# Optimization experiments

Measured on AMD Instinct MI355X. Metric: run time of the kernel, lower is better.

Reference implementation:

```python
import jax, jax.numpy as jnp
import numpy as np

N_NODES = 100000
N_EDGES = 1600000
IN_FEATS = 64
OUT_FEATS = 64
BN_EPS = 1e-5


def setup_inputs() -> dict:
    key = jax.random.key(0)
    ks = jax.random.split(key, 5)
    feats = jax.random.normal(ks[0], (N_NODES, IN_FEATS), dtype=jnp.float32)
    src = jax.random.randint(ks[1], (N_EDGES,), 0, N_NODES, dtype=jnp.int32)
    dst = jax.random.randint(ks[2], (N_EDGES,), 0, N_NODES, dtype=jnp.int32)
    scale = 1.0 / np.sqrt(IN_FEATS)
    W = jax.random.normal(ks[3], (IN_FEATS, OUT_FEATS), dtype=jnp.float32) * scale
    b = jnp.zeros((OUT_FEATS,), dtype=jnp.float32)
    Wr = jax.random.normal(ks[4], (IN_FEATS, OUT_FEATS), dtype=jnp.float32) * scale
    br = jnp.zeros((OUT_FEATS,), dtype=jnp.float32)
    gamma = jnp.ones((OUT_FEATS,), dtype=jnp.float32)
    beta = jnp.zeros((OUT_FEATS,), dtype=jnp.float32)
    return {"feats": feats, "src": src, "dst": dst, "W": W, "b": b,
            "Wr": Wr, "br": br, "gamma": gamma, "beta": beta}


def reference(feats, src, dst, W, b, Wr, br, gamma, beta):
    N = feats.shape[0]
    # GraphConv(norm='none'): sum-aggregate source features into destinations (SpMM),
    # then linear + bias + activation (relu).
    agg = jax.ops.segment_sum(feats[src], dst, num_segments=N)  # [N, IN]
    h = jax.nn.relu(agg @ W + b)                                # [N, OUT]
    # residual branch: activation(Linear(feats))
    res = jax.nn.relu(feats @ Wr + br)
    h = h + res
    # dropout p=0.0 -> identity
    # BatchNorm1d (training mode): biased variance over node dim, eps=1e-5
    mean = jnp.mean(h, axis=0)
    var = jnp.var(h, axis=0)
    return (h - mean) * jax.lax.rsqrt(var + BN_EPS) * gamma + beta
```

## Files before the change

### kernel.cpp

```cpp
#include <hip/hip_runtime.h>
#include <hip/hip_bf16.h>


typedef __attribute__((ext_vector_type(8))) short short8;
typedef __attribute__((ext_vector_type(4))) float f32x4;

constexpr int BKT  = 128;
constexpr int NBKT_MAX = 1024;
constexpr int SCAP = 3072;
constexpr int PB   = 8192;
constexpr int CAST_BLKS = 2048;

static __device__ __forceinline__ float bfbits_lo(unsigned u) {
    union { unsigned u; float f; } c; c.u = u << 16; return c.f;
}
static __device__ __forceinline__ float bfbits_hi(unsigned u) {
    union { unsigned u; float f; } c; c.u = u & 0xffff0000u; return c.f;
}
static __device__ __forceinline__ short bf16r(float x) {
    __hip_bfloat16 h = __float2bfloat16(x);
    union { __hip_bfloat16 h; short s; } c; c.h = h; return c.s;
}
static __device__ __forceinline__ unsigned bf16pair(float x, float y) {
    return (unsigned)(unsigned short)bf16r(x) | ((unsigned)(unsigned short)bf16r(y) << 16);
}

__global__ __launch_bounds__(256) void k_prep(
    const float* __restrict__ feats, unsigned short* __restrict__ feats_h, int total8,
    const float* __restrict__ W, const float* __restrict__ Wr,
    short* __restrict__ Wpk, short* __restrict__ Wrpk)
{
    const int bid = blockIdx.x;
    if (bid < CAST_BLKS) {
        for (int i = bid * 256 + threadIdx.x; i < total8; i += CAST_BLKS * 256) {
            float4 v0 = ((const float4*)feats)[i * 2];
            float4 v1 = ((const float4*)feats)[i * 2 + 1];
            short8 o;
            o[0] = bf16r(v0.x); o[1] = bf16r(v0.y); o[2] = bf16r(v0.z); o[3] = bf16r(v0.w);
            o[4] = bf16r(v1.x); o[5] = bf16r(v1.y); o[6] = bf16r(v1.z); o[7] = bf16r(v1.w);
            ((short8*)feats_h)[i] = o;
        }
    } else {
        for (int idx = threadIdx.x; idx < 8192; idx += 256) {
            const int m = idx >> 12;
            const int rem = idx & 4095;
            const int j = rem & 7;
            const int q = rem >> 3;
            const int lane = q & 63;
            const int st = q >> 6;
            const int s = st >> 2;
            const int t = st & 3;
            const int k = s * 32 + (lane >> 4) * 8 + j;
            const int n = t * 16 + (lane & 15);
            const float v = (m == 0) ? W[k * 64 + n] : Wr[k * 64 + n];
            short* out = (m == 0) ? Wpk : Wrpk;
            out[rem] = bf16r(v);
        }
    }
}

__global__ __launch_bounds__(1024) void k_part(
    const int* __restrict__ src, const int* __restrict__ dst,
    int* __restrict__ cursor, unsigned* __restrict__ pk_slots,
    int n_edges, int nbkt)
{
    __shared__ unsigned stage[PB];
    __shared__ int hist[NBKT_MAX], lofs[NBKT_MAX], cnt2[NBKT_MAX];
    const int tid = threadIdx.x;
    const int e0 = blockIdx.x * PB;

    for (int i = tid; i < NBKT_MAX; i += 1024) { hist[i] = 0; cnt2[i] = 0; }
    __syncthreads();

    unsigned pk[8]; unsigned short bb8[8];
    #pragma unroll
    for (int i = 0; i < 8; i++) {
        const int e = e0 + i * 1024 + tid;
        if (e < n_edges) {
            const int d = dst[e];
            const int s = src[e];
            const int bb = d >> 7;
            bb8[i] = (unsigned short)bb;
            pk[i] = ((unsigned)(d & 127) << 17) | (unsigned)s;
            atomicAdd(&hist[bb], 1);
        } else bb8[i] = 0xffff;
    }
    __syncthreads();

    int myc = 0, mybase = 0;
    if (tid < nbkt) {
        myc = hist[tid];
        if (myc > 0) mybase = atomicAdd(&cursor[tid], myc);
    }
    const int v = (tid < nbkt) ? myc : 0;
    lofs[tid] = v;
    __syncthreads();
    for (int off = 1; off < 1024; off <<= 1) {
        int x = (tid >= off) ? lofs[tid - off] : 0;
        __syncthreads();
        lofs[tid] += x;
        __syncthreads();
    }
    const int myex = lofs[tid] - v;
    __syncthreads();
    lofs[tid] = myex;
    __syncthreads();

    #pragma unroll
    for (int i = 0; i < 8; i++) {
        if (bb8[i] != 0xffff) {
            const int spos = lofs[bb8[i]] + atomicAdd(&cnt2[bb8[i]], 1);
            stage[spos] = pk[i];
        }
    }
    __syncthreads();

    if (tid < nbkt && myc > 0) {
        int room = SCAP - mybase;
        const int c = myc < room ? myc : (room > 0 ? room : 0);
        unsigned* gp = pk_slots + (size_t)tid * SCAP + mybase;
        const int lbase = myex;
        for (int j = 0; j < c; j++) gp[j] = stage[lbase + j];
    }
}

__global__ __launch_bounds__(1024) void k_gsort(
    const unsigned short* __restrict__ feats_h, const int* __restrict__ cursor,
    const unsigned* __restrict__ pk_slots, unsigned short* __restrict__ aggh,
    int n_nodes)
{
    __shared__ unsigned raw[SCAP];
    __shared__ unsigned srt[SCAP];
    __shared__ int cnt[BKT], cnt2[BKT], lofs[BKT], noff[BKT + 1];
    const int bkt = blockIdx.x;
    const int tid = threadIdx.x;
    int m = cursor[bkt]; if (m > SCAP) m = SCAP;
    const unsigned* gsl = pk_slots + (size_t)bkt * SCAP;

    if (tid < BKT) { cnt[tid] = 0; cnt2[tid] = 0; }
    __syncthreads();
    for (int i = tid; i < m; i += 1024) {
        const unsigned p = gsl[i];
        raw[i] = p;
        atomicAdd(&cnt[p >> 17], 1);
    }
    __syncthreads();
    if (tid < BKT) lofs[tid] = cnt[tid];
    __syncthreads();
    for (int off = 1; off < BKT; off <<= 1) {
        int x = 0;
        if (tid < BKT && tid >= off) x = lofs[tid - off];
        __syncthreads();
        if (tid < BKT) lofs[tid] += x;
        __syncthreads();
    }
    if (tid < BKT) noff[tid + 1] = lofs[tid];
    if (tid == 0) noff[0] = 0;
    __syncthreads();
    for (int i = tid; i < m; i += 1024) {
        const unsigned p = raw[i];
        const int d = p >> 17;
        const int spos = noff[d] + atomicAdd(&cnt2[d], 1);
        srt[spos] = p & 0x1ffffu;
    }
    __syncthreads();

    const int wave = tid >> 6;
    const int lane = tid & 63;
    const int half = lane >> 5;
    const int li   = lane & 31;
    #pragma unroll 1
    for (int k = 0; k < 8; k++) {
        const int nl = wave * 8 + k;
        const int n  = bkt * BKT + nl;
        if (n >= n_nodes) break;
        const int beg = noff[nl], end = noff[nl + 1];
        float ax0 = 0.f, ax1 = 0.f, ax2 = 0.f, ax3 = 0.f;
        float ay0 = 0.f, ay1 = 0.f, ay2 = 0.f, ay3 = 0.f;
        for (int base = beg; base < end; base += 16) {
            #pragma unroll
            for (int j = 0; j < 8; j++) {
                const int e = base + 2 * j + half;
                const bool vd = e < end;
                const unsigned s = srt[vd ? e : beg];
                const unsigned val = *(const unsigned*)(feats_h + (size_t)s * 64 + li * 2);
                const float flo = vd ? bfbits_lo(val) : 0.f;
                const float fhi = vd ? bfbits_hi(val) : 0.f;
                switch (j & 3) {
                    case 0: ax0 += flo; ay0 += fhi; break;
                    case 1: ax1 += flo; ay1 += fhi; break;
                    case 2: ax2 += flo; ay2 += fhi; break;
                    default: ax3 += flo; ay3 += fhi; break;
                }
            }
        }
        float ax = (ax0 + ax1) + (ax2 + ax3);
        float ay = (ay0 + ay1) + (ay2 + ay3);
        ax += __shfl_xor(ax, 32);
        ay += __shfl_xor(ay, 32);
        if (half == 0)
            *(unsigned*)(aggh + (size_t)n * 128 + li * 2) = bf16pair(ax, ay);
    }
}

__global__ __launch_bounds__(512) void k_mv(
    const unsigned short* aggh, const unsigned short* __restrict__ feats_h,
    const short* __restrict__ Wpk, const short* __restrict__ Wrpk,
    const float* __restrict__ b, const float* __restrict__ br,
    float* h, float* __restrict__ bnacc, int n_nodes)
{
    __shared__ float ssum[64], ssq[64];
    const int tid = threadIdx.x;
    const int wave = tid >> 6;
    const int lane = tid & 63;
    if (tid < 64) { ssum[tid] = 0.f; ssq[tid] = 0.f; }
    __syncthreads();

    short8 wf[8], wrf[8];
    #pragma unroll
    for (int i = 0; i < 8; i++) {
        wf[i]  = *(const short8*)(Wpk  + (i * 64 + lane) * 8);
        wrf[i] = *(const short8*)(Wrpk + (i * 64 + lane) * 8);
    }
    float bt[4], brt[4];
    #pragma unroll
    for (int t = 0; t < 4; t++) {
        bt[t]  = b [t * 16 + (lane & 15)];
        brt[t] = br[t * 16 + (lane & 15)];
    }

    const int r0 = blockIdx.x * 128 + wave * 16;
    int arow = r0 + (lane & 15);
    if (arow >= n_nodes) arow = n_nodes - 1;
    const int kb = (lane >> 4) * 8;

    short8 aggA[2], feaA[2];
    #pragma unroll
    for (int s = 0; s < 2; s++) {
        aggA[s] = *(const short8*)(aggh + (size_t)arow * 128 + s * 32 + kb);
        feaA[s] = *(const short8*)(feats_h + (size_t)arow * 64 + s * 32 + kb);
    }

    #pragma unroll
    for (int t = 0; t < 4; t++) {
        f32x4 c1 = {0.f, 0.f, 0.f, 0.f};
        f32x4 c2 = {0.f, 0.f, 0.f, 0.f};
        c1 = __builtin_amdgcn_mfma_f32_16x16x32_bf16(aggA[0], wf [t],     c1, 0, 0, 0);
        c1 = __builtin_amdgcn_mfma_f32_16x16x32_bf16(aggA[1], wf [4 + t], c1, 0, 0, 0);
        c2 = __builtin_amdgcn_mfma_f32_16x16x32_bf16(feaA[0], wrf[t],     c2, 0, 0, 0);
        c2 = __builtin_amdgcn_mfma_f32_16x16x32_bf16(feaA[1], wrf[4 + t], c2, 0, 0, 0);
        const int col = t * 16 + (lane & 15);
        float ls = 0.f, lq = 0.f;
        #pragma unroll
        for (int r = 0; r < 4; r++) {
            const int row = r0 + (lane >> 4) * 4 + r;
            const float hv = fmaxf(c1[r] + bt[t], 0.f) + fmaxf(c2[r] + brt[t], 0.f);
            if (row < n_nodes) {
                h[(size_t)row * 64 + col] = hv;
                ls += hv;
                lq += hv * hv;
            }
        }
        ls += __shfl_xor(ls, 16); ls += __shfl_xor(ls, 32);
        lq += __shfl_xor(lq, 16); lq += __shfl_xor(lq, 32);
        if ((lane >> 4) == 0) {
            atomicAdd(&ssum[col], ls);
            atomicAdd(&ssq[col], lq);
        }
    }
    __syncthreads();
    if (tid < 64) {
        atomicAdd(&bnacc[tid], ssum[tid]);
        atomicAdd(&bnacc[64 + tid], ssq[tid]);
    }
}

__global__ __launch_bounds__(256) void k_bnapply(
    float* __restrict__ h, const float* __restrict__ bnacc,
    const float* __restrict__ gamma, const float* __restrict__ beta,
    int total4, float inv_n)
{
    __shared__ float ssc[64], ssh[64];
    if (threadIdx.x < 64) {
        const int t = threadIdx.x;
        const float mean = bnacc[t] * inv_n;
        const float var  = bnacc[64 + t] * inv_n - mean * mean;
        const float sc = gamma[t] * rsqrtf(var + 1e-5f);
        ssc[t] = sc;
        ssh[t] = beta[t] - mean * sc;
    }
    __syncthreads();
    for (int i = blockIdx.x * blockDim.x + threadIdx.x; i < total4;
         i += gridDim.x * blockDim.x) {
        float4 v = ((float4*)h)[i];
        const int j = (i & 15) << 2;
        v.x = v.x * ssc[j + 0] + ssh[j + 0];
        v.y = v.y * ssc[j + 1] + ssh[j + 1];
        v.z = v.z * ssc[j + 2] + ssh[j + 2];
        v.w = v.w * ssc[j + 3] + ssh[j + 3];
        ((float4*)h)[i] = v;
    }
}

extern "C" void kernel_launch(void* const* d_in, const int* in_sizes, int n_in,
                              void* d_out, int out_size, void* d_ws, size_t ws_size,
                              hipStream_t stream)
{
    const float* feats = (const float*)d_in[0];
    const int*   src   = (const int*)  d_in[1];
    const int*   dst   = (const int*)  d_in[2];
    const float* W     = (const float*)d_in[3];
    const float* b     = (const float*)d_in[4];
    const float* Wr    = (const float*)d_in[5];
    const float* br    = (const float*)d_in[6];
    const float* gamma = (const float*)d_in[7];
    const float* beta  = (const float*)d_in[8];

    const int n_nodes = in_sizes[0] / 64;
    const int n_edges = in_sizes[1];
    const int nbkt    = (n_nodes + BKT - 1) / BKT;
    const int nbatch  = (n_edges + PB - 1) / PB;

    int*      cursor   = (int*)d_ws;
    float*    bnacc    = (float*)(cursor + NBKT_MAX);
    unsigned* pk_slots = (unsigned*)(bnacc + 128);
    unsigned short* feats_h = (unsigned short*)(pk_slots + (size_t)nbkt * SCAP);
    short*    Wpk      = (short*)(feats_h + (size_t)n_nodes * 64);
    short*    Wrpk     = Wpk + 4096;
    unsigned short* aggh = (unsigned short*)d_out;
    float*    h        = (float*)d_out;

    hipMemsetAsync(cursor, 0, (size_t)(NBKT_MAX + 128) * sizeof(int), stream);

    k_prep <<<CAST_BLKS + 1, 256, 0, stream>>>(feats, feats_h, n_nodes * 8,
                                               W, Wr, Wpk, Wrpk);
    k_part <<<nbatch, 1024, 0, stream>>>(src, dst, cursor, pk_slots, n_edges, nbkt);
    k_gsort<<<nbkt, 1024, 0, stream>>>(feats_h, cursor, pk_slots, aggh, n_nodes);
    k_mv   <<<(n_nodes + 127) / 128, 512, 0, stream>>>(aggh, feats_h, Wpk, Wrpk,
                                                       b, br, h, bnacc, n_nodes);
    k_bnapply<<<2048, 256, 0, stream>>>(h, bnacc, gamma, beta, n_nodes * 16,
                                        1.f / (float)n_nodes);
}
```

Baseline: 111.8 us.

## Fuse edge partitioning into prep kernel and halve gather bucket size

Merges the bf16 cast/weight-pack kernel and the edge partition kernel into one launch, so the cast and partition blocks run concurrently. The partition now scatters each edge straight to global bucket slots via atomics instead of staging through a shared-memory prefix scan. Buckets shrink from 128 to 64 nodes (512-thread gather blocks, twice as many), and the gather loop gets an unmasked fast path for full 16-edge chunks. Direct scattered global writes are less coalesced, and the smaller per-bucket capacity raises the chance of overflow truncation.

```diff
diff --git a/kernel.cpp b/kernel.cpp
--- a/kernel.cpp
+++ b/kernel.cpp
@@ -5,11 +5,11 @@
 typedef __attribute__((ext_vector_type(8))) short short8;
 typedef __attribute__((ext_vector_type(4))) float f32x4;
 
-constexpr int BKT  = 128;
-constexpr int NBKT_MAX = 1024;
-constexpr int SCAP = 3072;
+constexpr int BKT  = 64;
+constexpr int NBKT_MAX = 2048;
+constexpr int SCAP = 1536;
 constexpr int PB   = 8192;
-constexpr int CAST_BLKS = 2048;
+constexpr int CAST_BLKS = 800;
 
 static __device__ __forceinline__ float bfbits_lo(unsigned u) {
     union { unsigned u; float f; } c; c.u = u << 16; return c.f;
@@ -25,14 +25,52 @@
     return (unsigned)(unsigned short)bf16r(x) | ((unsigned)(unsigned short)bf16r(y) << 16);
 }
 
-__global__ __launch_bounds__(256) void k_prep(
+__global__ __launch_bounds__(1024) void k_prep_part(
+    const int* __restrict__ src, const int* __restrict__ dst,
+    int* __restrict__ cursor, unsigned* __restrict__ pk_slots,
+    int n_edges, int nbatch, int nbkt,
     const float* __restrict__ feats, unsigned short* __restrict__ feats_h, int total8,
     const float* __restrict__ W, const float* __restrict__ Wr,
     short* __restrict__ Wpk, short* __restrict__ Wrpk)
 {
+    __shared__ int hist[NBKT_MAX], basei[NBKT_MAX], cnt2[NBKT_MAX];
     const int bid = blockIdx.x;
-    if (bid < CAST_BLKS) {
-        for (int i = bid * 256 + threadIdx.x; i < total8; i += CAST_BLKS * 256) {
+    const int tid = threadIdx.x;
+    if (bid < nbatch) {
+        const int e0 = bid * PB;
+        for (int i = tid; i < nbkt; i += 1024) { hist[i] = 0; cnt2[i] = 0; }
+        __syncthreads();
+        unsigned pk[8]; unsigned short bb8[8];
+        #pragma unroll
+        for (int i = 0; i < 8; i++) {
+            const int e = e0 + i * 1024 + tid;
+            if (e < n_edges) {
+                const int d = dst[e];
+                const int s = src[e];
+                const int bb = d >> 6;
+                bb8[i] = (unsigned short)bb;
+                pk[i] = ((unsigned)(d & 63) << 17) | (unsigned)s;
+                atomicAdd(&hist[bb], 1);
+            } else bb8[i] = 0xffff;
+        }
+        __syncthreads();
+        for (int i = tid; i < nbkt; i += 1024) {
+            const int c = hist[i];
+            basei[i] = (c > 0) ? atomicAdd(&cursor[i], c) : 0;
+        }
+        __syncthreads();
+        #pragma unroll
+        for (int i = 0; i < 8; i++) {
+            if (bb8[i] != 0xffff) {
+                const int bb = bb8[i];
+                const int pos = basei[bb] + atomicAdd(&cnt2[bb], 1);
+                if (pos < SCAP)
+                    pk_slots[(size_t)bb * SCAP + pos] = pk[i];
+            }
+        }
+    } else if (bid < nbatch + CAST_BLKS) {
+        const int cb = bid - nbatch;
+        for (int i = cb * 1024 + tid; i < total8; i += CAST_BLKS * 1024) {
             float4 v0 = ((const float4*)feats)[i * 2];
             float4 v1 = ((const float4*)feats)[i * 2 + 1];
             short8 o;
@@ -41,7 +79,7 @@
             ((short8*)feats_h)[i] = o;
         }
     } else {
-        for (int idx = threadIdx.x; idx < 8192; idx += 256) {
+        for (int idx = tid; idx < 8192; idx += 1024) {
             const int m = idx >> 12;
             const int rem = idx & 4095;
             const int j = rem & 7;
@@ -59,72 +97,7 @@
     }
 }
 
-__global__ __launch_bounds__(1024) void k_part(
-    const int* __restrict__ src, const int* __restrict__ dst,
-    int* __restrict__ cursor, unsigned* __restrict__ pk_slots,
-    int n_edges, int nbkt)
-{
-    __shared__ unsigned stage[PB];
-    __shared__ int hist[NBKT_MAX], lofs[NBKT_MAX], cnt2[NBKT_MAX];
-    const int tid = threadIdx.x;
-    const int e0 = blockIdx.x * PB;
-
-    for (int i = tid; i < NBKT_MAX; i += 1024) { hist[i] = 0; cnt2[i] = 0; }
-    __syncthreads();
-
-    unsigned pk[8]; unsigned short bb8[8];
-    #pragma unroll
-    for (int i = 0; i < 8; i++) {
-        const int e = e0 + i * 1024 + tid;
-        if (e < n_edges) {
-            const int d = dst[e];
-            const int s = src[e];
-            const int bb = d >> 7;
-            bb8[i] = (unsigned short)bb;
-            pk[i] = ((unsigned)(d & 127) << 17) | (unsigned)s;
-            atomicAdd(&hist[bb], 1);
-        } else bb8[i] = 0xffff;
-    }
-    __syncthreads();
-
-    int myc = 0, mybase = 0;
-    if (tid < nbkt) {
-        myc = hist[tid];
-        if (myc > 0) mybase = atomicAdd(&cursor[tid], myc);
-    }
-    const int v = (tid < nbkt) ? myc : 0;
-    lofs[tid] = v;
-    __syncthreads();
-    for (int off = 1; off < 1024; off <<= 1) {
-        int x = (tid >= off) ? lofs[tid - off] : 0;
-        __syncthreads();
-        lofs[tid] += x;
-        __syncthreads();
-    }
-    const int myex = lofs[tid] - v;
-    __syncthreads();
-    lofs[tid] = myex;
-    __syncthreads();
-
-    #pragma unroll
-    for (int i = 0; i < 8; i++) {
-        if (bb8[i] != 0xffff) {
-            const int spos = lofs[bb8[i]] + atomicAdd(&cnt2[bb8[i]], 1);
-            stage[spos] = pk[i];
-        }
-    }
-    __syncthreads();
-
-    if (tid < nbkt && myc > 0) {
-        int room = SCAP - mybase;
-        const int c = myc < room ? myc : (room > 0 ? room : 0);
-        unsigned* gp = pk_slots + (size_t)tid * SCAP + mybase;
-        const int lbase = myex;
-        for (int j = 0; j < c; j++) gp[j] = stage[lbase + j];
-    }
-}
-
-__global__ __launch_bounds__(1024) void k_gsort(
+__global__ __launch_bounds__(512) void k_gsort(
     const unsigned short* __restrict__ feats_h, const int* __restrict__ cursor,
     const unsigned* __restrict__ pk_slots, unsigned short* __restrict__ aggh,
     int n_nodes)
@@ -139,7 +112,7 @@
 
     if (tid < BKT) { cnt[tid] = 0; cnt2[tid] = 0; }
     __syncthreads();
-    for (int i = tid; i < m; i += 1024) {
+    for (int i = tid; i < m; i += 512) {
         const unsigned p = gsl[i];
         raw[i] = p;
         atomicAdd(&cnt[p >> 17], 1);
@@ -157,11 +130,10 @@
     if (tid < BKT) noff[tid + 1] = lofs[tid];
     if (tid == 0) noff[0] = 0;
     __syncthreads();
-    for (int i = tid; i < m; i += 1024) {
+    for (int i = tid; i < m; i += 512) {
         const unsigned p = raw[i];
         const int d = p >> 17;
-        const int spos = noff[d] + atomicAdd(&cnt2[d], 1);
-        srt[spos] = p & 0x1ffffu;
+        srt[noff[d] + atomicAdd(&cnt2[d], 1)] = p & 0x1ffffu;
     }
     __syncthreads();
 
@@ -175,31 +147,35 @@
         const int n  = bkt * BKT + nl;
         if (n >= n_nodes) break;
         const int beg = noff[nl], end = noff[nl + 1];
-        float ax0 = 0.f, ax1 = 0.f, ax2 = 0.f, ax3 = 0.f;
-        float ay0 = 0.f, ay1 = 0.f, ay2 = 0.f, ay3 = 0.f;
-        for (int base = beg; base < end; base += 16) {
+        float ax[4] = {0.f, 0.f, 0.f, 0.f};
+        float ay[4] = {0.f, 0.f, 0.f, 0.f};
+        int base = beg;
+        for (; base + 16 <= end; base += 16) {
+            #pragma unroll
+            for (int j = 0; j < 8; j++) {
+                const unsigned s = srt[base + 2 * j + half];
+                const unsigned v = *(const unsigned*)(feats_h + (size_t)s * 64 + li * 2);
+                ax[j & 3] += bfbits_lo(v);
+                ay[j & 3] += bfbits_hi(v);
+            }
+        }
+        if (base < end) {
             #pragma unroll
             for (int j = 0; j < 8; j++) {
                 const int e = base + 2 * j + half;
                 const bool vd = e < end;
                 const unsigned s = srt[vd ? e : beg];
-                const unsigned val = *(const unsigned*)(feats_h + (size_t)s * 64 + li * 2);
-                const float flo = vd ? bfbits_lo(val) : 0.f;
-                const float fhi = vd ? bfbits_hi(val) : 0.f;
-                switch (j & 3) {
-                    case 0: ax0 += flo; ay0 += fhi; break;
-                    case 1: ax1 += flo; ay1 += fhi; break;
-                    case 2: ax2 += flo; ay2 += fhi; break;
-                    default: ax3 += flo; ay3 += fhi; break;
-                }
+                const unsigned v = *(const unsigned*)(feats_h + (size_t)s * 64 + li * 2);
+                ax[j & 3] += vd ? bfbits_lo(v) : 0.f;
+                ay[j & 3] += vd ? bfbits_hi(v) : 0.f;
             }
         }
-        float ax = (ax0 + ax1) + (ax2 + ax3);
-        float ay = (ay0 + ay1) + (ay2 + ay3);
-        ax += __shfl_xor(ax, 32);
-        ay += __shfl_xor(ay, 32);
+        float axs = (ax[0] + ax[1]) + (ax[2] + ax[3]);
+        float ays = (ay[0] + ay[1]) + (ay[2] + ay[3]);
+        axs += __shfl_xor(axs, 32);
+        ays += __shfl_xor(ays, 32);
         if (half == 0)
-            *(unsigned*)(aggh + (size_t)n * 128 + li * 2) = bf16pair(ax, ay);
+            *(unsigned*)(aggh + (size_t)n * 128 + li * 2) = bf16pair(axs, ays);
     }
 }
 
@@ -332,10 +308,10 @@
 
     hipMemsetAsync(cursor, 0, (size_t)(NBKT_MAX + 128) * sizeof(int), stream);
 
-    k_prep <<<CAST_BLKS + 1, 256, 0, stream>>>(feats, feats_h, n_nodes * 8,
-                                               W, Wr, Wpk, Wrpk);
-    k_part <<<nbatch, 1024, 0, stream>>>(src, dst, cursor, pk_slots, n_edges, nbkt);
-    k_gsort<<<nbkt, 1024, 0, stream>>>(feats_h, cursor, pk_slots, aggh, n_nodes);
+    k_prep_part<<<nbatch + CAST_BLKS + 1, 1024, 0, stream>>>(
+        src, dst, cursor, pk_slots, n_edges, nbatch, nbkt,
+        feats, feats_h, n_nodes * 8, W, Wr, Wpk, Wrpk);
+    k_gsort<<<nbkt, 512, 0, stream>>>(feats_h, cursor, pk_slots, aggh, n_nodes);
     k_mv   <<<(n_nodes + 127) / 128, 512, 0, stream>>>(aggh, feats_h, Wpk, Wrpk,
                                                        b, br, h, bnacc, n_nodes);
     k_bnapply<<<2048, 256, 0, stream>>>(h, bnacc, gamma, beta, n_nodes * 16,
```

Measured after the change: 103.2 us. -7.7%, faster.
